# Optimization experiments

Measured on AMD Instinct MI355X. Metric: run time of the kernel, lower is better.

Reference implementation:

```python
import jax, jax.numpy as jnp
import numpy as np

B, T, V, E, U, OUT = 1024, 64, 30, 128, 512, 20


def _lstm(x, W, Uh, b, reverse=False, return_seq=True):
    """Keras-style LSTM (gate order i,f,g,o). x: [B,T,D]. Returns [B,T,U] or [B,U]."""
    nu = Uh.shape[0]
    if reverse:
        x = x[:, ::-1]
    xz = jnp.einsum('btd,dg->btg', x, W) + b  # [B,T,4U] input projection, precomputed

    def step(carry, z_t):
        h, c = carry
        z = z_t + h @ Uh
        i, f, g, o = jnp.split(z, 4, axis=-1)
        c = jax.nn.sigmoid(f) * c + jax.nn.sigmoid(i) * jnp.tanh(g)
        h = jax.nn.sigmoid(o) * jnp.tanh(c)
        return (h, c), h

    bsz = x.shape[0]
    init = (jnp.zeros((bsz, nu), x.dtype), jnp.zeros((bsz, nu), x.dtype))
    (h_last, _), hs = jax.lax.scan(step, init, jnp.swapaxes(xz, 0, 1))
    if return_seq:
        hs = jnp.swapaxes(hs, 0, 1)  # [B,T,U]
        if reverse:
            hs = hs[:, ::-1]
        return hs
    return h_last


def setup_inputs() -> dict:
    key = jax.random.key(0)
    ks = jax.random.split(key, 14)
    f32 = jnp.float32

    def n(k, shape, s=0.05):
        return jax.random.normal(k, shape, f32) * s

    G = 4 * U
    return {
        'x': jax.random.randint(ks[0], (B, T), 0, V, dtype=jnp.int32),
        'emb': n(ks[1], (V, E)),
        # layer 1 forward / backward directions
        'W1f': n(ks[2], (E, G)), 'U1f': n(ks[3], (U, G)), 'b1f': jnp.zeros((G,), f32),
        'W1b': n(ks[4], (E, G)), 'U1b': n(ks[5], (U, G)), 'b1b': jnp.zeros((G,), f32),
        # layer 2 forward / backward directions (input dim = 2U from concat)
        'W2f': n(ks[6], (2 * U, G)), 'U2f': n(ks[7], (U, G)), 'b2f': jnp.zeros((G,), f32),
        'W2b': n(ks[8], (2 * U, G)), 'U2b': n(ks[9], (U, G)), 'b2b': jnp.zeros((G,), f32),
        # dense head
        'Wd': n(ks[10], (2 * U, 2 * U)), 'bd': jnp.zeros((2 * U,), f32),
        'Wo': n(ks[11], (2 * U, OUT)), 'bo': jnp.zeros((OUT,), f32),
    }


def reference(x, emb, W1f, U1f, b1f, W1b, U1b, b1b,
              W2f, U2f, b2f, W2b, U2b, b2b, Wd, bd, Wo, bo):
    e = emb[x]  # [B,T,E] embedding lookup
    # Bidirectional LSTM 1, return_sequences=True, concat merge -> [B,T,2U]
    h1 = jnp.concatenate([
        _lstm(e, W1f, U1f, b1f),
        _lstm(e, W1b, U1b, b1b, reverse=True),
    ], axis=-1)
    # Bidirectional LSTM 2, return_sequences=False -> [B,2U]
    h2 = jnp.concatenate([
        _lstm(h1, W2f, U2f, b2f, return_seq=False),
        _lstm(h1, W2b, U2b, b2b, reverse=True, return_seq=False),
    ], axis=-1)
    d = jax.nn.relu(h2 @ Wd + bd)  # Dense(2U, relu)
    return d @ Wo + bo             # Dense(output_len), [B,OUT]
```

## Files before the change

kernel.cpp:

```cpp
#include <hip/hip_runtime.h>
#include <hip/hip_bf16.h>

typedef __hip_bfloat16 bf16;
typedef __attribute__((ext_vector_type(4))) float f32x4;
typedef __attribute__((ext_vector_type(8))) short s16x8;

__device__ __forceinline__ float sigf(float x) {
    return 1.0f / (1.0f + __expf(-x));
}
__device__ __forceinline__ float tanh_f(float x) {
    float ax = fabsf(x);
    float e = __expf(-2.0f * ax);
    float r = (1.0f - e) / (1.0f + e);
    return x < 0.0f ? -r : r;
}

#define GLL16(src, ldst)                                                      \
    __builtin_amdgcn_global_load_lds(                                         \
        (const __attribute__((address_space(1))) void*)(src),                 \
        (__attribute__((address_space(3))) void*)(ldst), 16, 0, 0)

__global__ void k_embw(const float* __restrict__ emb,
                       const float* __restrict__ W1f, const float* __restrict__ b1f,
                       const float* __restrict__ W1b, const float* __restrict__ b1b,
                       float* __restrict__ embW) {
    int c = blockIdx.x * 256 + threadIdx.x;
    int v = blockIdx.y;
    int d = blockIdx.z;
    const float* W = d ? W1b : W1f;
    const float* b = d ? b1b : b1f;
    float acc = b[c];
    const float* er = emb + v * 128;
#pragma unroll 8
    for (int e = 0; e < 128; ++e) acc += er[e] * W[e * 2048 + c];
    int n = ((c & 511) << 2) | (c >> 9);
    embW[(d * 30 + v) * 2048 + n] = acc;
}

__global__ void k_b2r(const float* __restrict__ b2f, const float* __restrict__ b2b,
                      float* __restrict__ dst) {
    int i = blockIdx.x * 256 + threadIdx.x;
    int d = i >> 11, n = i & 2047;
    int c = ((n & 3) << 9) | (n >> 2);
    dst[i] = (d ? b2b : b2f)[c];
}

__global__ void k_trans_all(const float* __restrict__ U1f, const float* __restrict__ U1b,
                            const float* __restrict__ W2f, const float* __restrict__ U2f,
                            const float* __restrict__ W2b, const float* __restrict__ U2b,
                            const float* __restrict__ Wd,
                            bf16* __restrict__ Ut1, bf16* __restrict__ BigBt,
                            bf16* __restrict__ Wdt) {
    int l = blockIdx.x;
    const float* src; bf16* dst;
    int BX, ncols, kpitch, koff, reorder;
    if (l < 256)       { l -= 0;    src = U1f; dst = Ut1;               BX = 8;  ncols = 2048; kpitch = 512;  koff = 0;    reorder = 1; }
    else if (l < 512)  { l -= 256;  src = U1b; dst = Ut1 + 2048 * 512;  BX = 8;  ncols = 2048; kpitch = 512;  koff = 0;    reorder = 1; }
    else if (l < 1024) { l -= 512;  src = W2f; dst = BigBt;             BX = 16; ncols = 2048; kpitch = 1536; koff = 0;    reorder = 1; }
    else if (l < 1280) { l -= 1024; src = U2f; dst = BigBt;             BX = 8;  ncols = 2048; kpitch = 1536; koff = 1024; reorder = 1; }
    else if (l < 1792) { l -= 1280; src = W2b; dst = BigBt + (size_t)2048 * 1536; BX = 16; ncols = 2048; kpitch = 1536; koff = 0;    reorder = 1; }
    else if (l < 2048) { l -= 1792; src = U2b; dst = BigBt + (size_t)2048 * 1536; BX = 8;  ncols = 2048; kpitch = 1536; koff = 1024; reorder = 1; }
    else               { l -= 2048; src = Wd;  dst = Wdt;               BX = 16; ncols = 1024; kpitch = 1024; koff = 0;    reorder = 0; }
    const int k0 = (l % BX) * 64;
    const int c0 = (l / BX) * 64;

    __shared__ float tile[64][65];
    const int tid = threadIdx.x;
#pragma unroll
    for (int i = 0; i < 16; ++i) {
        int seg = tid + i * 256;
        int r = seg >> 6, cc = seg & 63;
        tile[r][cc] = src[(size_t)(k0 + r) * ncols + c0 + cc];
    }
    __syncthreads();
#pragma unroll
    for (int i = 0; i < 16; ++i) {
        int seg = tid + i * 256;
        int nl = seg >> 6, kl = seg & 63;
        int c = c0 + nl;
        int n = reorder ? (((c & 511) << 2) | (c >> 9)) : c;
        int kabs = koff + k0 + kl;
        dst[(size_t)n * kpitch + (kabs ^ ((n & 7) << 3))] =
            __float2bfloat16(tile[kl][nl]);
    }
}

template<int MODE>
__global__ __launch_bounds__(256, 2)
void k_step(const bf16* __restrict__ A1, const bf16* __restrict__ A2,
            const bf16* __restrict__ Bt, const float* __restrict__ table,
            const int* __restrict__ xin, float* __restrict__ c_st,
            bf16* __restrict__ h_out, bf16* __restrict__ h1s, int t)
{
    constexpr int NCH = (MODE == 0) ? 8 : 24;
    constexpr int BP  = (MODE == 0) ? 512 : 1536;

    __shared__ __align__(16) short ldss[24576];

    const int tid  = threadIdx.x;
    const int lane = tid & 63;
    const int wv   = tid >> 6;
    const int wm   = wv << 5;

    const int xcd = blockIdx.x & 7, idx = blockIdx.x >> 3;
    const int n0  = ((xcd << 2) | (idx >> 4)) << 6;
    const int m0  = (idx & 15) << 7;

    const int dir = (m0 >= 1024);
    const int t_a = dir ? 63 - t : t;
    const int rl  = lane & 15;
    const int q8  = (lane >> 4) << 3;
    const int q4  = (lane >> 4) << 2;
    const int xk  = (rl & 7) << 3;
    const int u0  = n0 >> 2;
    const bool rec = (t > 0);

    const char* a1b;
    if constexpr (MODE == 1)
        a1b = (const char*)(A1 + ((size_t)t_a << 20) + ((size_t)(m0 & 1023) << 10));
    else
        a1b = (const char*)(A1 + (size_t)m0 * 512);
    const char* const btb = (const char*)(Bt + ((size_t)dir * 2048 + n0) * BP);
    const char* const a2b = (const char*)A2;

    auto stage = [&](int c, int buf) {
        char* base = (char*)ldss + buf * 24576;
#pragma unroll
        for (int i = 0; i < 4; ++i) {
            const int u = i * 256 + tid;
            const int r = u >> 3, j = u & 7;
            const char* src;
            if constexpr (MODE == 0)
                src = a1b + r * 1024 + c * 128 + j * 16;
            else
                src = (c < 16) ? a1b + r * 2048 + c * 128 + j * 16
                               : a2b + (size_t)(m0 + r) * 1024 + (c - 16) * 128 + j * 16;
            GLL16(src, base + (i * 256 + wv * 64) * 16);
        }
#pragma unroll
        for (int i = 0; i < 2; ++i) {
            const int u = i * 256 + tid;
            const int r = u >> 3, j = u & 7;
            GLL16(btb + (size_t)r * (BP * 2) + c * 128 + j * 16,
                  base + 16384 + (i * 256 + wv * 64) * 16);
        }
    };

    f32x4 acc[2][4];
#pragma unroll
    for (int i = 0; i < 2; ++i)
#pragma unroll
        for (int j = 0; j < 4; ++j) acc[i][j] = (f32x4){0.f, 0.f, 0.f, 0.f};

    auto compute = [&](int buf) {
        const short* as = ldss + buf * 12288;
        const short* bs = as + 8192;
#pragma unroll
        for (int ks = 0; ks < 2; ++ks) {
            const int eo = ((ks << 5) + q8) ^ xk;
            s16x8 af[2], bq[4];
#pragma unroll
            for (int f = 0; f < 2; ++f)
                af[f] = *(const s16x8*)&as[(wm + f * 16 + rl) * 64 + eo];
#pragma unroll
            for (int f = 0; f < 4; ++f)
                bq[f] = *(const s16x8*)&bs[(f * 16 + rl) * 64 + eo];
#pragma unroll
            for (int fm = 0; fm < 2; ++fm)
#pragma unroll
                for (int fn = 0; fn < 4; ++fn)
                    acc[fm][fn] = __builtin_amdgcn_mfma_f32_16x16x32_bf16(
                        af[fm], bq[fn], acc[fm][fn], 0, 0, 0);
        }
    };

    if constexpr (MODE == 0) {
        if (rec) {
            stage(0, 0);
            for (int c = 0; c < NCH; ++c) {
                __syncthreads();
                if (c + 1 < NCH) stage(c + 1, (c + 1) & 1);
                compute(c & 1);
            }
        }
    } else {
        const int nch = rec ? 24 : 16;
        stage(0, 0);
        for (int c = 0; c < 16; ++c) {
            __syncthreads();
            if (c + 1 < nch) stage(c + 1, (c + 1) & 1);
            compute(c & 1);
        }
        if (rec) {
            for (int c = 16; c < 24; ++c) {
                __syncthreads();
                if (c + 1 < 24) stage(c + 1, (c + 1) & 1);
                compute(c & 1);
            }
        }
    }

    float* z = (float*)ldss;
    __syncthreads();
#pragma unroll
    for (int fm = 0; fm < 2; ++fm)
#pragma unroll
        for (int fn = 0; fn < 4; ++fn) {
            const int zr = wm + fm * 16 + q4;
            const int zc = fn * 16 + rl;
#pragma unroll
            for (int r = 0; r < 4; ++r)
                z[(zr + r) * 68 + zc] = acc[fm][fn][r];
        }
    __syncthreads();
#pragma unroll 2
    for (int j = 0; j < 8; ++j) {
        const int cid = j * 256 + tid;
        const int ml = cid >> 4;
        const int ul = cid & 15;
        const int mg = m0 + ml;
        const int b  = mg & 1023;
        float4 z4 = *(float4*)&z[ml * 68 + (ul << 2)];
        const float* tab;
        if constexpr (MODE == 0) {
            const int v = xin[(b << 6) + t_a];
            tab = table + (size_t)(dir * 30 + v) * 2048;
        } else {
            tab = table + dir * 2048;
        }
        const float4 tv = *(const float4*)&tab[n0 + (ul << 2)];
        const float zi = z4.x + tv.x, zf = z4.y + tv.y;
        const float zg = z4.z + tv.z, zo = z4.w + tv.w;
        const float ig = sigf(zi), fg = sigf(zf);
        const float gg = tanh_f(zg), og = sigf(zo);
        const int u = u0 + ul;
        const size_t cu = (size_t)mg * 512 + u;
        const float cv = rec ? c_st[cu] : 0.0f;
        const float cn = fg * cv + ig * gg;
        c_st[cu] = cn;
        const float h = og * tanh_f(cn);
        const int us = u ^ ((mg & 7) << 3);
        h_out[(size_t)mg * 512 + us] = __float2bfloat16(h);
        if constexpr (MODE == 0) {
            const int col = (((dir << 9) | u) ^ ((b & 7) << 3));
            h1s[(((size_t)t_a << 10) + b) * 1024 + col] = __float2bfloat16(h);
        }
    }
}

__global__ __launch_bounds__(256, 2)
void k_dense(const bf16* __restrict__ hin, const bf16* __restrict__ Bt,
             const float* __restrict__ bd, bf16* __restrict__ dbuf)
{
    __shared__ __align__(16) short ldss[32768];
    const int tid  = threadIdx.x;
    const int lane = tid & 63;
    const int wv   = tid >> 6;
    const int wm   = (wv >> 1) << 6;
    const int wn   = (wv & 1) << 6;
    const int n0   = (blockIdx.x & 7) << 7;
    const int m0   = (blockIdx.x >> 3) << 7;

    const char* const a1b = (const char*)(hin + (size_t)m0 * 512);
    const char* const a2b = (const char*)(hin + (size_t)1024 * 512);
    const char* const btb = (const char*)(Bt + (size_t)n0 * 1024);

    auto stage = [&](int c, int buf) {
#pragma unroll
        for (int i = 0; i < 4; ++i) {
            const int u = i * 256 + tid;
            const int r = u >> 3, j = u & 7;
            const char* src = (c < 8)
                ? a1b + r * 1024 + c * 128 + j * 16
                : a2b + (size_t)(m0 + r) * 1024 + (c - 8) * 128 + j * 16;
            GLL16(src, (char*)ldss + buf * 16384 + (i * 256 + wv * 64) * 16);
        }
#pragma unroll
        for (int i = 0; i < 4; ++i) {
            const int u = i * 256 + tid;
            const int r = u >> 3, j = u & 7;
            GLL16(btb + (size_t)r * 2048 + c * 128 + j * 16,
                  (char*)ldss + 32768 + buf * 16384 + (i * 256 + wv * 64) * 16);
        }
    };

    f32x4 acc[4][4];
#pragma unroll
    for (int i = 0; i < 4; ++i)
#pragma unroll
        for (int j = 0; j < 4; ++j) acc[i][j] = (f32x4){0.f, 0.f, 0.f, 0.f};

    stage(0, 0);
    const int rl = lane & 15;
    const int q8 = (lane >> 4) << 3;
    const int xk = (rl & 7) << 3;

#pragma unroll 2
    for (int c = 0; c < 16; ++c) {
        __syncthreads();
        if (c + 1 < 16) stage(c + 1, (c + 1) & 1);
        const short* as = ldss + (c & 1) * 8192;
        const short* bs = ldss + 16384 + (c & 1) * 8192;
#pragma unroll
        for (int ks = 0; ks < 2; ++ks) {
            const int eo = ((ks << 5) + q8) ^ xk;
            s16x8 af[4], bq[4];
#pragma unroll
            for (int f = 0; f < 4; ++f)
                af[f] = *(const s16x8*)&as[(wm + f * 16 + rl) * 64 + eo];
#pragma unroll
            for (int f = 0; f < 4; ++f)
                bq[f] = *(const s16x8*)&bs[(wn + f * 16 + rl) * 64 + eo];
#pragma unroll
            for (int fm = 0; fm < 4; ++fm)
#pragma unroll
                for (int fn = 0; fn < 4; ++fn)
                    acc[fm][fn] = __builtin_amdgcn_mfma_f32_16x16x32_bf16(
                        af[fm], bq[fn], acc[fm][fn], 0, 0, 0);
        }
    }

#pragma unroll
    for (int fn = 0; fn < 4; ++fn) {
        const int col = n0 + wn + fn * 16 + rl;
        const float bdv = bd[col];
#pragma unroll
        for (int fm = 0; fm < 4; ++fm) {
            const int rb = m0 + wm + fm * 16 + ((lane >> 4) << 2);
#pragma unroll
            for (int r = 0; r < 4; ++r) {
                float v = acc[fm][fn][r] + bdv;
                dbuf[(size_t)(rb + r) * 1024 + col] =
                    __float2bfloat16(v > 0.f ? v : 0.f);
            }
        }
    }
}

__global__ __launch_bounds__(256)
void k_out(const bf16* __restrict__ dbuf, const float* __restrict__ Wo,
           const float* __restrict__ bo, float* __restrict__ out) {
    int b = blockIdx.x, tid = threadIdx.x;
    int wv = tid >> 6, lane = tid & 63;
    float acc[5] = {0.f, 0.f, 0.f, 0.f, 0.f};
    for (int kk = 0; kk < 1024; kk += 64) {
        float a = __bfloat162float(dbuf[b * 1024 + kk + lane]);
#pragma unroll
        for (int j = 0; j < 5; ++j)
            acc[j] += a * Wo[(kk + lane) * 20 + wv + j * 4];
    }
#pragma unroll
    for (int j = 0; j < 5; ++j) {
        float s = acc[j];
        for (int off = 32; off; off >>= 1) s += __shfl_down(s, off, 64);
        if (lane == 0) out[b * 20 + wv + j * 4] = s + bo[wv + j * 4];
    }
}

extern "C" void kernel_launch(void* const* d_in, const int* in_sizes, int n_in,
                              void* d_out, int out_size, void* d_ws, size_t ws_size,
                              hipStream_t stream) {
    const int*   x   = (const int*)  d_in[0];
    const float* emb = (const float*)d_in[1];
    const float* W1f = (const float*)d_in[2];
    const float* U1f = (const float*)d_in[3];
    const float* b1f = (const float*)d_in[4];
    const float* W1b = (const float*)d_in[5];
    const float* U1b = (const float*)d_in[6];
    const float* b1b = (const float*)d_in[7];
    const float* W2f = (const float*)d_in[8];
    const float* U2f = (const float*)d_in[9];
    const float* b2f = (const float*)d_in[10];
    const float* W2b = (const float*)d_in[11];
    const float* U2b = (const float*)d_in[12];
    const float* b2b = (const float*)d_in[13];
    const float* Wd  = (const float*)d_in[14];
    const float* bd  = (const float*)d_in[15];
    const float* Wo  = (const float*)d_in[16];
    const float* bo  = (const float*)d_in[17];

    char* ws = (char*)d_ws;
    float* embW = (float*)(ws + 0);
    float* b2r  = (float*)(ws + 491520);
    bf16* Ut1   = (bf16*)(ws + 507904);
    bf16* BigBt = (bf16*)(ws + 4702208);
    bf16* Wdt   = (bf16*)(ws + 17285120);
    bf16* hA    = (bf16*)(ws + 19382272);
    bf16* hB    = (bf16*)(ws + 21479424);
    float* cst  = (float*)(ws + 23576576);
    bf16* dbuf  = (bf16*)(ws + 27770880);
    bf16* h1seq = (bf16*)(ws + 29868032);

    k_embw<<<dim3(8, 30, 2), 256, 0, stream>>>(emb, W1f, b1f, W1b, b1b, embW);
    k_b2r<<<16, 256, 0, stream>>>(b2f, b2b, b2r);
    k_trans_all<<<2304, 256, 0, stream>>>(U1f, U1b, W2f, U2f, W2b, U2b, Wd,
                                          Ut1, BigBt, Wdt);

    bf16 *hin = hA, *hout = hB;
    for (int t = 0; t < 64; ++t) {
        k_step<0><<<512, 256, 0, stream>>>(
            hin, (const bf16*)nullptr, Ut1, embW, x, cst, hout, h1seq, t);
        bf16* tmp = hin; hin = hout; hout = tmp;
    }

    for (int t = 0; t < 64; ++t) {
        k_step<1><<<512, 256, 0, stream>>>(
            h1seq, hin, BigBt, b2r, (const int*)nullptr, cst, hout,
            (bf16*)nullptr, t);
        bf16* tmp = hin; hin = hout; hout = tmp;
    }

    k_dense<<<64, 256, 0, stream>>>(hin, Wdt, bd, dbuf);
    k_out<<<1024, 256, 0, stream>>>(dbuf, Wo, bo, (float*)d_out);
}
```

Measured before the change: 2.193 ms.

## Make each LSTM layer a persistent kernel with per-row-group atomic flag barriers

Replaces the 64 per-timestep kernel launches per layer with one persistent kernel per layer that loops over all timesteps. Blocks sharing an M row group sync through global atomic counters (32 arrivals per step) instead of kernel boundaries, which removes launch overhead and the full-grid drain. The design assumes all 512 blocks are co-resident (2 per CU) and uses a bounded spin with a timeout, so it risks deadlock or silent wrong results if occupancy is lower. Flags reuse the dbuf workspace region and are cleared with a memset before each layer.

```diff
diff --git a/kernel.cpp b/kernel.cpp
--- a/kernel.cpp
+++ b/kernel.cpp
@@ -87,13 +87,13 @@
 
 template<int MODE>
 __global__ __launch_bounds__(256, 2)
-void k_step(const bf16* __restrict__ A1, const bf16* __restrict__ A2,
-            const bf16* __restrict__ Bt, const float* __restrict__ table,
-            const int* __restrict__ xin, float* __restrict__ c_st,
-            bf16* __restrict__ h_out, bf16* __restrict__ h1s, int t)
+void k_layer(const bf16* __restrict__ A1g, const bf16* __restrict__ Bt,
+             const float* __restrict__ table, const int* __restrict__ xin,
+             float* __restrict__ c_st, bf16* __restrict__ hA,
+             bf16* __restrict__ hB, bf16* __restrict__ h1s,
+             int* __restrict__ flags)
 {
-    constexpr int NCH = (MODE == 0) ? 8 : 24;
-    constexpr int BP  = (MODE == 0) ? 512 : 1536;
+    constexpr int BP = (MODE == 0) ? 512 : 1536;
 
     __shared__ __align__(16) short ldss[24576];
 
@@ -104,146 +104,172 @@
 
     const int xcd = blockIdx.x & 7, idx = blockIdx.x >> 3;
     const int n0  = ((xcd << 2) | (idx >> 4)) << 6;
-    const int m0  = (idx & 15) << 7;
+    const int mg  = idx & 15;
+    const int m0  = mg << 7;
 
     const int dir = (m0 >= 1024);
-    const int t_a = dir ? 63 - t : t;
     const int rl  = lane & 15;
     const int q8  = (lane >> 4) << 3;
     const int q4  = (lane >> 4) << 2;
     const int xk  = (rl & 7) << 3;
     const int u0  = n0 >> 2;
-    const bool rec = (t > 0);
-
-    const char* a1b;
-    if constexpr (MODE == 1)
-        a1b = (const char*)(A1 + ((size_t)t_a << 20) + ((size_t)(m0 & 1023) << 10));
-    else
-        a1b = (const char*)(A1 + (size_t)m0 * 512);
+
     const char* const btb = (const char*)(Bt + ((size_t)dir * 2048 + n0) * BP);
-    const char* const a2b = (const char*)A2;
-
-    auto stage = [&](int c, int buf) {
-        char* base = (char*)ldss + buf * 24576;
-#pragma unroll
-        for (int i = 0; i < 4; ++i) {
-            const int u = i * 256 + tid;
-            const int r = u >> 3, j = u & 7;
-            const char* src;
-            if constexpr (MODE == 0)
-                src = a1b + r * 1024 + c * 128 + j * 16;
-            else
-                src = (c < 16) ? a1b + r * 2048 + c * 128 + j * 16
-                               : a2b + (size_t)(m0 + r) * 1024 + (c - 16) * 128 + j * 16;
-            GLL16(src, base + (i * 256 + wv * 64) * 16);
-        }
-#pragma unroll
-        for (int i = 0; i < 2; ++i) {
-            const int u = i * 256 + tid;
-            const int r = u >> 3, j = u & 7;
-            GLL16(btb + (size_t)r * (BP * 2) + c * 128 + j * 16,
-                  base + 16384 + (i * 256 + wv * 64) * 16);
-        }
-    };
-
-    f32x4 acc[2][4];
-#pragma unroll
-    for (int i = 0; i < 2; ++i)
-#pragma unroll
-        for (int j = 0; j < 4; ++j) acc[i][j] = (f32x4){0.f, 0.f, 0.f, 0.f};
-
-    auto compute = [&](int buf) {
-        const short* as = ldss + buf * 12288;
-        const short* bs = as + 8192;
-#pragma unroll
-        for (int ks = 0; ks < 2; ++ks) {
-            const int eo = ((ks << 5) + q8) ^ xk;
-            s16x8 af[2], bq[4];
-#pragma unroll
-            for (int f = 0; f < 2; ++f)
-                af[f] = *(const s16x8*)&as[(wm + f * 16 + rl) * 64 + eo];
-#pragma unroll
-            for (int f = 0; f < 4; ++f)
-                bq[f] = *(const s16x8*)&bs[(f * 16 + rl) * 64 + eo];
-#pragma unroll
-            for (int fm = 0; fm < 2; ++fm)
-#pragma unroll
-                for (int fn = 0; fn < 4; ++fn)
-                    acc[fm][fn] = __builtin_amdgcn_mfma_f32_16x16x32_bf16(
-                        af[fm], bq[fn], acc[fm][fn], 0, 0, 0);
-        }
-    };
-
-    if constexpr (MODE == 0) {
+
+#pragma unroll 1
+    for (int s = 0; s < 64; ++s) {
+        const bool rec = (s > 0);
         if (rec) {
+            __syncthreads();
+            if (tid == 0) {
+                int* f = &flags[((s - 1) << 4) + mg];
+                __hip_atomic_fetch_add(f, 1, __ATOMIC_RELEASE,
+                                       __HIP_MEMORY_SCOPE_AGENT);
+                int it = 0;
+                while (__hip_atomic_load(f, __ATOMIC_RELAXED,
+                                         __HIP_MEMORY_SCOPE_AGENT) < 32 &&
+                       it < 200000) {
+                    __builtin_amdgcn_s_sleep(8);
+                    ++it;
+                }
+                (void)__hip_atomic_load(f, __ATOMIC_ACQUIRE,
+                                        __HIP_MEMORY_SCOPE_AGENT);
+            }
+            __syncthreads();
+        }
+
+        const int t_a = dir ? 63 - s : s;
+        const bf16* hin  = (s & 1) ? hB : hA;
+        bf16*       hout = (s & 1) ? hA : hB;
+        const char* a1b;
+        if constexpr (MODE == 1)
+            a1b = (const char*)(A1g + ((size_t)t_a << 20) + ((size_t)(m0 & 1023) << 10));
+        else
+            a1b = (const char*)(hin + (size_t)m0 * 512);
+        const char* const a2b = (const char*)hin;
+
+        auto stage = [&](int c, int buf) {
+            char* base = (char*)ldss + buf * 24576;
+#pragma unroll
+            for (int i = 0; i < 4; ++i) {
+                const int u = i * 256 + tid;
+                const int r = u >> 3, j = u & 7;
+                const char* src;
+                if constexpr (MODE == 0)
+                    src = a1b + r * 1024 + c * 128 + j * 16;
+                else
+                    src = (c < 16) ? a1b + r * 2048 + c * 128 + j * 16
+                                   : a2b + (size_t)(m0 + r) * 1024 + (c - 16) * 128 + j * 16;
+                GLL16(src, base + (i * 256 + wv * 64) * 16);
+            }
+#pragma unroll
+            for (int i = 0; i < 2; ++i) {
+                const int u = i * 256 + tid;
+                const int r = u >> 3, j = u & 7;
+                GLL16(btb + (size_t)r * (BP * 2) + c * 128 + j * 16,
+                      base + 16384 + (i * 256 + wv * 64) * 16);
+            }
+        };
+
+        f32x4 acc[2][4];
+#pragma unroll
+        for (int i = 0; i < 2; ++i)
+#pragma unroll
+            for (int j = 0; j < 4; ++j) acc[i][j] = (f32x4){0.f, 0.f, 0.f, 0.f};
+
+        auto compute = [&](int buf) {
+            const short* as = ldss + buf * 12288;
+            const short* bs = as + 8192;
+#pragma unroll
+            for (int ks = 0; ks < 2; ++ks) {
+                const int eo = ((ks << 5) + q8) ^ xk;
+                s16x8 af[2], bq[4];
+#pragma unroll
+                for (int f = 0; f < 2; ++f)
+                    af[f] = *(const s16x8*)&as[(wm + f * 16 + rl) * 64 + eo];
+#pragma unroll
+                for (int f = 0; f < 4; ++f)
+                    bq[f] = *(const s16x8*)&bs[(f * 16 + rl) * 64 + eo];
+#pragma unroll
+                for (int fm = 0; fm < 2; ++fm)
+#pragma unroll
+                    for (int fn = 0; fn < 4; ++fn)
+                        acc[fm][fn] = __builtin_amdgcn_mfma_f32_16x16x32_bf16(
+                            af[fm], bq[fn], acc[fm][fn], 0, 0, 0);
+            }
+        };
+
+        if constexpr (MODE == 0) {
+            if (rec) {
+                stage(0, 0);
+                for (int c = 0; c < 8; ++c) {
+                    __syncthreads();
+                    if (c + 1 < 8) stage(c + 1, (c + 1) & 1);
+                    compute(c & 1);
+                }
+            }
+        } else {
+            const int nch = rec ? 24 : 16;
             stage(0, 0);
-            for (int c = 0; c < NCH; ++c) {
+            for (int c = 0; c < 16; ++c) {
                 __syncthreads();
-                if (c + 1 < NCH) stage(c + 1, (c + 1) & 1);
+                if (c + 1 < nch) stage(c + 1, (c + 1) & 1);
                 compute(c & 1);
             }
-        }
-    } else {
-        const int nch = rec ? 24 : 16;
-        stage(0, 0);
-        for (int c = 0; c < 16; ++c) {
-            __syncthreads();
-            if (c + 1 < nch) stage(c + 1, (c + 1) & 1);
-            compute(c & 1);
-        }
-        if (rec) {
-            for (int c = 16; c < 24; ++c) {
-                __syncthreads();
-                if (c + 1 < 24) stage(c + 1, (c + 1) & 1);
-                compute(c & 1);
-            }
-        }
-    }
-
-    float* z = (float*)ldss;
-    __syncthreads();
-#pragma unroll
-    for (int fm = 0; fm < 2; ++fm)
-#pragma unroll
-        for (int fn = 0; fn < 4; ++fn) {
-            const int zr = wm + fm * 16 + q4;
-            const int zc = fn * 16 + rl;
-#pragma unroll
-            for (int r = 0; r < 4; ++r)
-                z[(zr + r) * 68 + zc] = acc[fm][fn][r];
-        }
-    __syncthreads();
+            if (rec) {
+                for (int c = 16; c < 24; ++c) {
+                    __syncthreads();
+                    if (c + 1 < 24) stage(c + 1, (c + 1) & 1);
+                    compute(c & 1);
+                }
+            }
+        }
+
+        float* z = (float*)ldss;
+        __syncthreads();
+#pragma unroll
+        for (int fm = 0; fm < 2; ++fm)
+#pragma unroll
+            for (int fn = 0; fn < 4; ++fn) {
+                const int zr = wm + fm * 16 + q4;
+                const int zc = fn * 16 + rl;
+#pragma unroll
+                for (int r = 0; r < 4; ++r)
+                    z[(zr + r) * 68 + zc] = acc[fm][fn][r];
+            }
+        __syncthreads();
 #pragma unroll 2
-    for (int j = 0; j < 8; ++j) {
-        const int cid = j * 256 + tid;
-        const int ml = cid >> 4;
-        const int ul = cid & 15;
-        const int mg = m0 + ml;
-        const int b  = mg & 1023;
-        float4 z4 = *(float4*)&z[ml * 68 + (ul << 2)];
-        const float* tab;
-        if constexpr (MODE == 0) {
-            const int v = xin[(b << 6) + t_a];
-            tab = table + (size_t)(dir * 30 + v) * 2048;
-        } else {
-            tab = table + dir * 2048;
-        }
-        const float4 tv = *(const float4*)&tab[n0 + (ul << 2)];
-        const float zi = z4.x + tv.x, zf = z4.y + tv.y;
-        const float zg = z4.z + tv.z, zo = z4.w + tv.w;
-        const float ig = sigf(zi), fg = sigf(zf);
-        const float gg = tanh_f(zg), og = sigf(zo);
-        const int u = u0 + ul;
-        const size_t cu = (size_t)mg * 512 + u;
-        const float cv = rec ? c_st[cu] : 0.0f;
-        const float cn = fg * cv + ig * gg;
-        c_st[cu] = cn;
-        const float h = og * tanh_f(cn);
-        const int us = u ^ ((mg & 7) << 3);
-        h_out[(size_t)mg * 512 + us] = __float2bfloat16(h);
-        if constexpr (MODE == 0) {
-            const int col = (((dir << 9) | u) ^ ((b & 7) << 3));
-            h1s[(((size_t)t_a << 10) + b) * 1024 + col] = __float2bfloat16(h);
+        for (int j = 0; j < 8; ++j) {
+            const int cid = j * 256 + tid;
+            const int ml = cid >> 4;
+            const int ul = cid & 15;
+            const int mgr = m0 + ml;
+            const int b  = mgr & 1023;
+            float4 z4 = *(float4*)&z[ml * 68 + (ul << 2)];
+            const float* tab;
+            if constexpr (MODE == 0) {
+                const int v = xin[(b << 6) + t_a];
+                tab = table + (size_t)(dir * 30 + v) * 2048;
+            } else {
+                tab = table + dir * 2048;
+            }
+            const float4 tv = *(const float4*)&tab[n0 + (ul << 2)];
+            const float zi = z4.x + tv.x, zf = z4.y + tv.y;
+            const float zg = z4.z + tv.z, zo = z4.w + tv.w;
+            const float ig = sigf(zi), fg = sigf(zf);
+            const float gg = tanh_f(zg), og = sigf(zo);
+            const int u = u0 + ul;
+            const size_t cu = (size_t)mgr * 512 + u;
+            const float cv = rec ? c_st[cu] : 0.0f;
+            const float cn = fg * cv + ig * gg;
+            c_st[cu] = cn;
+            const float h = og * tanh_f(cn);
+            const int us = u ^ ((mgr & 7) << 3);
+            hout[(size_t)mgr * 512 + us] = __float2bfloat16(h);
+            if constexpr (MODE == 0) {
+                const int col = (((dir << 9) | u) ^ ((b & 7) << 3));
+                h1s[(((size_t)t_a << 10) + b) * 1024 + col] = __float2bfloat16(h);
+            }
         }
     }
 }
@@ -390,26 +416,21 @@
     float* cst  = (float*)(ws + 23576576);
     bf16* dbuf  = (bf16*)(ws + 27770880);
     bf16* h1seq = (bf16*)(ws + 29868032);
+    int*  flags = (int*)(ws + 27770880);
 
     k_embw<<<dim3(8, 30, 2), 256, 0, stream>>>(emb, W1f, b1f, W1b, b1b, embW);
     k_b2r<<<16, 256, 0, stream>>>(b2f, b2b, b2r);
     k_trans_all<<<2304, 256, 0, stream>>>(U1f, U1b, W2f, U2f, W2b, U2b, Wd,
                                           Ut1, BigBt, Wdt);
 
-    bf16 *hin = hA, *hout = hB;
-    for (int t = 0; t < 64; ++t) {
-        k_step<0><<<512, 256, 0, stream>>>(
-            hin, (const bf16*)nullptr, Ut1, embW, x, cst, hout, h1seq, t);
-        bf16* tmp = hin; hin = hout; hout = tmp;
-    }
-
-    for (int t = 0; t < 64; ++t) {
-        k_step<1><<<512, 256, 0, stream>>>(
-            h1seq, hin, BigBt, b2r, (const int*)nullptr, cst, hout,
-            (bf16*)nullptr, t);
-        bf16* tmp = hin; hin = hout; hout = tmp;
-    }
-
-    k_dense<<<64, 256, 0, stream>>>(hin, Wdt, bd, dbuf);
+    (void)hipMemsetAsync(flags, 0, 4096, stream);
+    k_layer<0><<<512, 256, 0, stream>>>((const bf16*)nullptr, Ut1, embW, x,
+                                        cst, hA, hB, h1seq, flags);
+
+    (void)hipMemsetAsync(flags, 0, 4096, stream);
+    k_layer<1><<<512, 256, 0, stream>>>(h1seq, BigBt, b2r, (const int*)nullptr,
+                                        cst, hA, hB, (bf16*)nullptr, flags);
+
+    k_dense<<<64, 256, 0, stream>>>(hA, Wdt, bd, dbuf);
     k_out<<<1024, 256, 0, stream>>>(dbuf, Wo, bo, (float*)d_out);
 }
```

After: 6.834 ms. 212% more time.
